# Optimization experiments

Measured on AMD Instinct MI355X. Metric: run time of the kernel, lower is better.

Reference implementation:

```python
import jax, jax.numpy as jnp
import numpy as np

NUM_LABELS = 32
EMB = 128          # label_embedding_dim
HID = 1024         # hidden_dim (== encoder feature dim)
B, S = 128, 512


def setup_inputs() -> dict:
    key = jax.random.key(0)
    ks = jax.random.split(key, 8)
    k = 1.0 / np.sqrt(HID)  # torch GRU/Linear default init bound
    u = lambda kk, shape: jax.random.uniform(kk, shape, jnp.float32, minval=-k, maxval=k)
    return {
        "hidden_states": jax.random.normal(ks[0], (B, S, HID), jnp.float32),
        "emb": jax.random.normal(ks[1], (NUM_LABELS, EMB), jnp.float32),  # nn.Embedding ~ N(0,1)
        "W_ih": u(ks[2], (3 * HID, EMB + HID)),  # GRU input weights, gate order r,z,n
        "W_hh": u(ks[3], (3 * HID, HID)),
        "b_ih": u(ks[4], (3 * HID,)),
        "b_hh": u(ks[5], (3 * HID,)),
        "W_out": u(ks[6], (NUM_LABELS, HID)),
        "b_out": u(ks[7], (NUM_LABELS,)),
    }


def reference(hidden_states, emb, W_ih, W_hh, b_ih, b_hh, W_out, b_out):
    batch = hidden_states.shape[0]
    h0 = jnp.zeros((batch, W_hh.shape[1]), hidden_states.dtype)
    lab0 = jnp.broadcast_to(emb[0], (batch, emb.shape[1]))  # label_start_embedding (id 0)

    def step(carry, x_t):
        h, lab = carry
        inp = jnp.concatenate([x_t, lab], axis=-1)            # [B, HID+EMB]
        gi = inp @ W_ih.T + b_ih                               # [B, 3*HID]
        gh = h @ W_hh.T + b_hh
        ir, iz, in_ = jnp.split(gi, 3, axis=-1)
        hr, hz, hn = jnp.split(gh, 3, axis=-1)
        r = jax.nn.sigmoid(ir + hr)
        z = jax.nn.sigmoid(iz + hz)
        n = jnp.tanh(in_ + r * hn)
        h_new = (1.0 - z) * n + z * h                          # PyTorch GRU update
        logit = h_new @ W_out.T + b_out                        # dropout is identity in eval
        pred = jnp.argmax(logit, axis=-1)                      # softmax is monotone; argmax(probs)==argmax(logit)
        return (h_new, emb[pred]), logit

    xs = jnp.swapaxes(hidden_states, 0, 1)                     # [S, B, HID]
    _, logits = jax.lax.scan(step, (h0, lab0), xs)             # logits: [S, B, L]
    return jnp.swapaxes(logits, 0, 1)                          # [B, S, L]
```

## Files before the change

### kernel.cpp

```cpp
#include <hip/hip_runtime.h>


#define S_    512
#define HID_  1024
#define EMB_  128
#define NL_   32
#define G3_   3072

#define LDS_A_STRIDE 1032
#define LDS_A_BYTES  (48 * LDS_A_STRIDE * 2)
#define CP_STRIDE    52
#define LDS_CP_BYTES (4 * 64 * CP_STRIDE * 4)
#define LDS_BYTES    (LDS_A_BYTES + LDS_CP_BYTES)

typedef __attribute__((ext_vector_type(8))) short          short8;
typedef __attribute__((ext_vector_type(8))) unsigned short u16x8;
typedef __attribute__((ext_vector_type(4))) unsigned short u16x4;
typedef __attribute__((ext_vector_type(4))) float          f32x4;
typedef unsigned long long u64_t;

__device__ unsigned int   g_ctr[576];
__device__ unsigned int   g_flag[1];
__device__ unsigned int   g_vis[256];
__device__ unsigned int   g_hseq[2][64 * 16];
__device__ unsigned int   g_predw[128 * 16];
__device__ unsigned short g_hhi[2][128 * HID_];
__device__ unsigned short g_hlo[2][128 * HID_];
__device__ float          g_hf32[2][128 * HID_];
__device__ float          g_Glab[NL_ * G3_];
__device__ unsigned short g_Wlox[G3_ * HID_];
__device__ unsigned short g_Wlohh[G3_ * HID_];
__device__ float          g_GIXall[(size_t)S_ * 128 * 64 * 48];

__device__ __forceinline__ float bf2f(unsigned short u) {
  union { unsigned int i; float f; } v; v.i = ((unsigned int)u) << 16; return v.f;
}
__device__ __forceinline__ unsigned short f2bf(float f) {
  union { float f; unsigned int i; } v; v.f = f;
  unsigned int u = v.i;
  return (unsigned short)((u + 0x7FFFu + ((u >> 16) & 1u)) >> 16);
}
__device__ __forceinline__ short8 ld_bf8(const unsigned short* p) {
  return __builtin_bit_cast(short8, *(const u16x8*)p);
}
__device__ __forceinline__ float ldin(const void* p, long i, int f32) {
  return f32 ? ((const float*)p)[i] : bf2f(((const unsigned short*)p)[i]);
}
__device__ __forceinline__ void store_out(void* out, int f32, long idx, float v) {
  if (f32) ((float*)out)[idx] = v;
  else     ((unsigned short*)out)[idx] = f2bf(v);
}

__device__ __forceinline__ u64_t ald64(const void* p) {
  return __hip_atomic_load((const u64_t*)p, __ATOMIC_RELAXED,
                           __HIP_MEMORY_SCOPE_AGENT);
}
__device__ __forceinline__ void ast64(void* p, u64_t v) {
  __hip_atomic_store((u64_t*)p, v, __ATOMIC_RELAXED,
                     __HIP_MEMORY_SCOPE_AGENT);
}
__device__ __forceinline__ unsigned int ald32(const unsigned int* p) {
  return __hip_atomic_load(p, __ATOMIC_RELAXED, __HIP_MEMORY_SCOPE_AGENT);
}
__device__ __forceinline__ void ast32(unsigned int* p, unsigned int v) {
  __hip_atomic_store(p, v, __ATOMIC_RELAXED, __HIP_MEMORY_SCOPE_AGENT);
}
__device__ __forceinline__ short8 ld_bf8_coh(const unsigned short* p) {
  union { u64_t q[2]; short8 s; } u;
  u.q[0] = ald64(p);
  u.q[1] = ald64(p + 4);
  return u.s;
}
__device__ __forceinline__ f32x4 ld_f4_coh(const float* p) {
  union { u64_t q[2]; f32x4 f; } u;
  u.q[0] = ald64(p);
  u.q[1] = ald64(p + 2);
  return u.f;
}
__device__ __forceinline__ void st_f4_coh(float* p, f32x4 v) {
  union { f32x4 f; u64_t q[2]; } u; u.f = v;
  ast64(p, u.q[0]);
  ast64(p + 2, u.q[1]);
}
__device__ __forceinline__ void st_h4_coh(unsigned short* p, u16x4 v) {
  union { u16x4 h; u64_t q; } u; u.h = v;
  ast64(p, u.q);
}

__global__ void k_zero() {
  int t = blockIdx.x * 256 + threadIdx.x;
  if (t < 576) g_ctr[t] = 0u;
  else if (t < 832) g_vis[t - 576] = 0u;
  if (t >= 2048 && t < 4096) ((unsigned int*)g_hseq)[t - 2048] = 0u;
  if (t >= 4096 && t < 6144) g_predw[t - 4096] = 0u;
  const u16x4 z4 = {0, 0, 0, 0};
  const f32x4 zf = {0.f, 0.f, 0.f, 0.f};
  for (int i = t; i < 2 * 128 * HID_ / 4; i += 65536) {
    ((u16x4*)g_hhi)[i] = z4;
    ((u16x4*)g_hlo)[i] = z4;
    ((f32x4*)g_hf32)[i] = zf;
  }
}

__global__ void k_detect(const unsigned short* __restrict__ W) {
  unsigned bad = 0;
  for (int i = threadIdx.x; i < 1024; i += 64) {
    float v = bf2f(W[i]);
    if (!(v * v <= 1.0f)) bad = 1;
  }
  unsigned long long b = __ballot(bad != 0);
  if (threadIdx.x == 0) g_flag[0] = (b != 0ull) ? 1u : 0u;
}

__global__ void k_prep(const void* __restrict__ emb,
                       const void* __restrict__ W_ih,
                       const void* __restrict__ b_ih) {
  const int f32 = (int)g_flag[0];
  int l = blockIdx.x / 12;
  int n = (blockIdx.x % 12) * 256 + threadIdx.x;
  double acc = (double)ldin(b_ih, n, f32);
  for (int e = 0; e < EMB_; ++e)
    acc += (double)ldin(emb, (long)l * EMB_ + e, f32) *
           (double)ldin(W_ih, (long)n * (HID_ + EMB_) + HID_ + e, f32);
  g_Glab[l * G3_ + n] = (float)acc;
}

__global__ void k_prepw(const void* __restrict__ W_ih,
                        const void* __restrict__ W_hh) {
  if (!g_flag[0]) return;
  long i4 = ((long)blockIdx.x * 256 + threadIdx.x) * 4;
  if (i4 >= (long)G3_ * HID_) return;
  int row = (int)(i4 >> 10), col = (int)(i4 & 1023);
  f32x4 wh = *(const f32x4*)&((const float*)W_hh)[(long)row * HID_ + col];
  f32x4 wx = *(const f32x4*)&((const float*)W_ih)[(long)row * (HID_ + EMB_) + col];
  u16x4 lh, lx;
  #pragma unroll
  for (int j = 0; j < 4; ++j) {
    unsigned short h1 = f2bf(wh[j]);
    lh[j] = f2bf(wh[j] - bf2f(h1));
    unsigned short x1 = f2bf(wx[j]);
    lx[j] = f2bf(wx[j] - bf2f(x1));
  }
  *(u16x4*)&g_Wlohh[i4] = lh;
  *(u16x4*)&g_Wlox[i4]  = lx;
}

__device__ __forceinline__ void gridbar(int wg, int bar) {
  __syncthreads();
  if (threadIdx.x == 0) {
    asm volatile("s_waitcnt vmcnt(0)" ::: "memory");
    unsigned int* c1   = g_ctr + (wg & 7) * 64;
    unsigned int* root = g_ctr + 512;
    unsigned int old = __hip_atomic_fetch_add(c1, 1u, __ATOMIC_RELAXED,
                                              __HIP_MEMORY_SCOPE_AGENT);
    if (old == 32u * (unsigned)(bar + 1) - 1u)
      __hip_atomic_fetch_add(root, 1u, __ATOMIC_RELAXED,
                             __HIP_MEMORY_SCOPE_AGENT);
    unsigned int tgt = 8u * (unsigned)(bar + 1);
    while (__hip_atomic_load(root, __ATOMIC_RELAXED,
                             __HIP_MEMORY_SCOPE_AGENT) < tgt)
      __builtin_amdgcn_s_sleep(1);
  }
  __syncthreads();
}

__device__ __forceinline__ void wait_hseq(int half, int it) {
  if (threadIdx.x < 64) {
    const unsigned int* p = &g_hseq[half][threadIdx.x * 16];
    while ((int)ald32(p) < it) { }
  }
  __builtin_amdgcn_sched_barrier(0);
  __syncthreads();
}

__device__ __forceinline__ void stage_w(unsigned short* sA, const void* Wsrc,
                                        int wstride, int rg, int f32, int tid) {
  if (f32) {
    const float* Ws = (const float*)Wsrc;
    for (int i = tid; i < 48 * 1024 / 4; i += 256) {
      int e = i * 4, row = e >> 10, k4 = e & 1023;
      int grow = (row >> 4) * HID_ + rg * 16 + (row & 15);
      f32x4 v = *(const f32x4*)&Ws[(long)grow * wstride + k4];
      u16x4 o;
      #pragma unroll
      for (int j = 0; j < 4; ++j) o[j] = f2bf(v[j]);
      *(u16x4*)&sA[row * LDS_A_STRIDE + k4] = o;
    }
  } else {
    const unsigned short* Ws = (const unsigned short*)Wsrc;
    for (int i = tid; i < 48 * 1024 / 4; i += 256) {
      int e = i * 4, row = e >> 10, k4 = e & 1023;
      int grow = (row >> 4) * HID_ + rg * 16 + (row & 15);
      *(u16x4*)&sA[row * LDS_A_STRIDE + k4] =
          *(const u16x4*)&Ws[(long)grow * wstride + k4];
    }
  }
}

__global__ __launch_bounds__(256) void k_seq(
    const void* __restrict__ hs,
    const void* __restrict__ W_ih,
    const void* __restrict__ W_hh,
    const void* __restrict__ b_hh,
    const void* __restrict__ W_out,
    const void* __restrict__ b_out,
    void* __restrict__ out) {
  extern __shared__ char smem[];
  unsigned short* sA  = (unsigned short*)smem;
  float*          sCp = (float*)(smem + LDS_A_BYTES);

  const int f32 = (int)g_flag[0];
  const int tid = threadIdx.x;
  const int wg  = blockIdx.x;
  const bool isx = (wg < 128);
  const int lid  = isx ? wg : wg - 128;
  const int rg = lid >> 1, bg = lid & 1;
  const int slot = lid;
  const int lane = tid & 63, wv = tid >> 6;
  const int m = lane & 15, q = lane >> 4;
  const int bl = tid & 63;
  const int jj = (tid >> 6) * 4;
  const int kw0 = wv * 256 + q * 8;

  int bar = 0;

  if (tid == 0) ast32(&g_vis[wg], (unsigned)wg + 1u);
  gridbar(wg, bar); ++bar;
  if (tid == 0) {
    unsigned p = ((unsigned)wg + 37u) & 255u;
    if (ald32(&g_vis[p]) != p + 1u) store_out(out, f32, wg, 999.0f);
  }

  {
    const int slot0 = wg & 127;
    const int rg0 = slot0 >> 1, bg0 = slot0 & 1;
    stage_w(sA, W_ih, HID_ + EMB_, rg0, f32, tid);
    __syncthreads();
    const long bstride = (long)S_ * HID_;
    const long boffb = (long)(bg0 * 64) * S_ * HID_;
    for (int t = 0; t < 256; ++t) {
      const int it = ((wg >> 7) << 8) | t;
      f32x4 acc[3][4];
      #pragma unroll
      for (int rt = 0; rt < 3; ++rt)
        #pragma unroll
        for (int bt = 0; bt < 4; ++bt) acc[rt][bt] = f32x4{0.f, 0.f, 0.f, 0.f};
      const long boff = boffb + (long)it * HID_;
      if (f32) {
        const float* Bf = (const float*)hs + boff;
        #pragma unroll
        for (int kb = 0; kb < 8; ++kb) {
          const int k = kw0 + kb * 32;
          short8 avh[3];
          #pragma unroll
          for (int rt = 0; rt < 3; ++rt)
            avh[rt] = ld_bf8(&sA[(rt * 16 + m) * LDS_A_STRIDE + k]);
          short8 bxh[4], bxl[4];
          #pragma unroll
          for (int bt = 0; bt < 4; ++bt) {
            const float* bp = Bf + (long)(bt * 16 + m) * bstride + k;
            f32x4 x0 = *(const f32x4*)bp;
            f32x4 x1 = *(const f32x4*)(bp + 4);
            u16x8 th, tl;
            #pragma unroll
            for (int j = 0; j < 4; ++j) {
              unsigned short u0 = f2bf(x0[j]);
              th[j] = u0; tl[j] = f2bf(x0[j] - bf2f(u0));
              unsigned short u1 = f2bf(x1[j]);
              th[4 + j] = u1; tl[4 + j] = f2bf(x1[j] - bf2f(u1));
            }
            bxh[bt] = __builtin_bit_cast(short8, th);
            bxl[bt] = __builtin_bit_cast(short8, tl);
          }
          short8 avl[3];
          #pragma unroll
          for (int rt = 0; rt < 3; ++rt)
            avl[rt] = ld_bf8(&g_Wlox[(long)(rt * HID_ + rg0 * 16 + m) * HID_ + k]);
          #pragma unroll
          for (int rt = 0; rt < 3; ++rt)
            #pragma unroll
            for (int bt = 0; bt < 4; ++bt) {
              acc[rt][bt] = __builtin_amdgcn_mfma_f32_16x16x32_bf16(
                  avh[rt], bxh[bt], acc[rt][bt], 0, 0, 0);
              acc[rt][bt] = __builtin_amdgcn_mfma_f32_16x16x32_bf16(
                  avh[rt], bxl[bt], acc[rt][bt], 0, 0, 0);
              acc[rt][bt] = __builtin_amdgcn_mfma_f32_16x16x32_bf16(
                  avl[rt], bxh[bt], acc[rt][bt], 0, 0, 0);
              acc[rt][bt] = __builtin_amdgcn_mfma_f32_16x16x32_bf16(
                  avl[rt], bxl[bt], acc[rt][bt], 0, 0, 0);
            }
        }
      } else {
        const unsigned short* Bh = (const unsigned short*)hs + boff;
        #pragma unroll
        for (int kb = 0; kb < 8; ++kb) {
          const int k = kw0 + kb * 32;
          short8 avh[3], bxh[4];
          #pragma unroll
          for (int rt = 0; rt < 3; ++rt)
            avh[rt] = ld_bf8(&sA[(rt * 16 + m) * LDS_A_STRIDE + k]);
          #pragma unroll
          for (int bt = 0; bt < 4; ++bt)
            bxh[bt] = ld_bf8(&Bh[(long)(bt * 16 + m) * bstride + k]);
          #pragma unroll
          for (int rt = 0; rt < 3; ++rt)
            #pragma unroll
            for (int bt = 0; bt < 4; ++bt)
              acc[rt][bt] = __builtin_amdgcn_mfma_f32_16x16x32_bf16(
                  avh[rt], bxh[bt], acc[rt][bt], 0, 0, 0);
        }
      }
      __syncthreads();
      #pragma unroll
      for (int rt = 0; rt < 3; ++rt)
        #pragma unroll
        for (int bt = 0; bt < 4; ++bt)
          *(f32x4*)&sCp[(wv * 64 + bt * 16 + m) * CP_STRIDE + rt * 16 + q * 4] =
              acc[rt][bt];
      __syncthreads();
      #pragma unroll
      for (int g = 0; g < 3; ++g) {
        f32x4 sv = f32x4{0.f, 0.f, 0.f, 0.f};
        #pragma unroll
        for (int w = 0; w < 4; ++w)
          sv += *(const f32x4*)&sCp[(w * 64 + bl) * CP_STRIDE + g * 16 + jj];
        *(f32x4*)&g_GIXall[(((long)it * 128 + slot0) * 64 + bl) * 48 +
                           g * 16 + jj] = sv;
      }
      __syncthreads();
    }
  }
  __threadfence();
  gridbar(wg, bar); ++bar;

  if (!isx) stage_w(sA, W_hh, HID_, rg, f32, tid);
  __syncthreads();

  float bo = 0.f;
  if (isx && tid < 32) bo = ldin(b_out, tid, f32);
  f32x4 bhh[3];
  if (!isx) {
    const int jbase = rg * 16 + jj;
    #pragma unroll
    for (int g = 0; g < 3; ++g)
      #pragma unroll
      for (int t = 0; t < 4; ++t)
        bhh[g][t] = ldin(b_hh, (long)g * HID_ + jbase + t, f32);
  }

  float hreg[4] = {0.f, 0.f, 0.f, 0.f};
  f32x4 sred[3];

  for (int it = 0; it <= S_; ++it) {
    if (isx && it >= 1) {
      wait_hseq(wg >> 6, it);
      const int rb = (it + 1) & 1;
      if (it == 1 && wg == 0 && tid == 0) {
        float s = 0.f;
        for (int i = 0; i < 16; ++i) {
          union { u64_t q; float f[2]; } u; u.q = ald64(&g_hf32[0][2 * i]);
          s += u.f[0] * u.f[0] + u.f[1] * u.f[1];
        }
        if (s == 0.f) store_out(out, f32, 300, 555.0f);
      }
      const int b = wg, s = it - 1;
      float* scrp  = sCp;
      float* shrow = sCp + 256;
      {
        f32x4 hv = ld_f4_coh(&g_hf32[rb][(long)b * HID_ + tid * 4]);
        *(f32x4*)&shrow[(tid >> 5) * 132 + (tid & 31) * 4] = hv;
      }
      __syncthreads();
      {
        int l = tid >> 3, kc = tid & 7;
        const float* hr = shrow + kc * 132;
        float p = 0.f;
        if (f32) {
          const float* wr = (const float*)W_out + (long)l * HID_ + kc * 128;
          for (int k = 0; k < 128; k += 4) {
            f32x4 wa = *(const f32x4*)&wr[k];
            f32x4 ha = *(const f32x4*)&hr[k];
            #pragma unroll
            for (int j = 0; j < 4; ++j) p += wa[j] * ha[j];
          }
        } else {
          const unsigned short* wr =
              (const unsigned short*)W_out + (long)l * HID_ + kc * 128;
          for (int k = 0; k < 128; k += 8) {
            u16x8 w8 = *(const u16x8*)&wr[k];
            f32x4 ha = *(const f32x4*)&hr[k];
            f32x4 hb = *(const f32x4*)&hr[k + 4];
            #pragma unroll
            for (int j = 0; j < 4; ++j) {
              p += bf2f(w8[j]) * ha[j];
              p += bf2f(w8[4 + j]) * hb[j];
            }
          }
        }
        scrp[tid] = p;
      }
      __syncthreads();
      if (tid < 32) {
        const float* pp = sCp + tid * 8;
        float v = pp[0] + pp[1] + pp[2] + pp[3] + pp[4] + pp[5] + pp[6] + pp[7]
                  + bo;
        store_out(out, f32, ((long)b * S_ + s) * NL_ + tid, v);
        float bv = v; int bi = tid;
        #pragma unroll
        for (int off = 16; off; off >>= 1) {
          float v2 = __shfl_down(bv, off, 32);
          int   i2 = __shfl_down(bi, off, 32);
          if (v2 > bv || (v2 == bv && i2 < bi)) { bv = v2; bi = i2; }
        }
        if (tid == 0) ast32(&g_predw[b * 16], ((unsigned)it << 8) | (unsigned)bi);
      }
      __syncthreads();
    }

    if (!isx && it < S_) {
      f32x4 gixp[3];
      #pragma unroll
      for (int g = 0; g < 3; ++g)
        gixp[g] = *(const f32x4*)&g_GIXall[(((long)it * 128 + slot) * 64 + bl)
                                           * 48 + g * 16 + jj];

      wait_hseq(bg, it);
      const int rb = (it + 1) & 1;
      const int wb = it & 1;

      f32x4 acc[3][4];
      #pragma unroll
      for (int rt = 0; rt < 3; ++rt)
        #pragma unroll
        for (int bt = 0; bt < 4; ++bt) acc[rt][bt] = f32x4{0.f, 0.f, 0.f, 0.f};

      const unsigned short* Bhi = g_hhi[rb] + (long)(bg * 64) * HID_;
      const unsigned short* Blo = g_hlo[rb] + (long)(bg * 64) * HID_;
      #pragma unroll
      for (int kb = 0; kb < 8; ++kb) {
        const int k = kw0 + kb * 32;
        short8 avh[3], bh[4], blv[4];
        #pragma unroll
        for (int rt = 0; rt < 3; ++rt)
          avh[rt] = ld_bf8(&sA[(rt * 16 + m) * LDS_A_STRIDE + k]);
        #pragma unroll
        for (int bt = 0; bt < 4; ++bt) {
          bh[bt]  = ld_bf8_coh(&Bhi[(long)(bt * 16 + m) * HID_ + k]);
          blv[bt] = ld_bf8_coh(&Blo[(long)(bt * 16 + m) * HID_ + k]);
        }
        #pragma unroll
        for (int rt = 0; rt < 3; ++rt)
          #pragma unroll
          for (int bt = 0; bt < 4; ++bt) {
            acc[rt][bt] = __builtin_amdgcn_mfma_f32_16x16x32_bf16(
                avh[rt], bh[bt], acc[rt][bt], 0, 0, 0);
            acc[rt][bt] = __builtin_amdgcn_mfma_f32_16x16x32_bf16(
                avh[rt], blv[bt], acc[rt][bt], 0, 0, 0);
          }
        if (f32) {
          short8 avl[3];
          #pragma unroll
          for (int rt = 0; rt < 3; ++rt)
            avl[rt] = ld_bf8(&g_Wlohh[(long)(rt * HID_ + rg * 16 + m) * HID_ + k]);
          #pragma unroll
          for (int rt = 0; rt < 3; ++rt)
            #pragma unroll
            for (int bt = 0; bt < 4; ++bt) {
              acc[rt][bt] = __builtin_amdgcn_mfma_f32_16x16x32_bf16(
                  avl[rt], bh[bt], acc[rt][bt], 0, 0, 0);
              acc[rt][bt] = __builtin_amdgcn_mfma_f32_16x16x32_bf16(
                  avl[rt], blv[bt], acc[rt][bt], 0, 0, 0);
            }
        }
      }

      __syncthreads();
      #pragma unroll
      for (int rt = 0; rt < 3; ++rt)
        #pragma unroll
        for (int bt = 0; bt < 4; ++bt)
          *(f32x4*)&sCp[(wv * 64 + bt * 16 + m) * CP_STRIDE + rt * 16 + q * 4] =
              acc[rt][bt];
      __syncthreads();
      #pragma unroll
      for (int g = 0; g < 3; ++g) {
        f32x4 sv = f32x4{0.f, 0.f, 0.f, 0.f};
        #pragma unroll
        for (int w = 0; w < 4; ++w)
          sv += *(const f32x4*)&sCp[(w * 64 + bl) * CP_STRIDE + g * 16 + jj];
        sred[g] = sv;
      }

      const int bglob = bg * 64 + bl;
      int pb = 0;
      if (it >= 1) {
        const unsigned int* pw = &g_predw[bglob * 16];
        unsigned w = ald32(pw);
        while ((int)(w >> 8) < it) { w = ald32(pw); }
        pb = (int)(w & 255u);
      }
      __builtin_amdgcn_sched_barrier(0);

      const int jbase = rg * 16 + jj;
      const float* gl = g_Glab + (long)pb * G3_;
      f32x4 glab[3];
      #pragma unroll
      for (int g = 0; g < 3; ++g)
        glab[g] = *(const f32x4*)&gl[g * HID_ + jbase];
      u16x4 whi, wlo;
      f32x4 hf;
      #pragma unroll
      for (int t4 = 0; t4 < 4; ++t4) {
        float ghr = sred[0][t4] + bhh[0][t4];
        float ghz = sred[1][t4] + bhh[1][t4];
        float ghn = sred[2][t4] + bhh[2][t4];
        float gir = gixp[0][t4] + glab[0][t4];
        float giz = gixp[1][t4] + glab[1][t4];
        float gin = gixp[2][t4] + glab[2][t4];
        float r = 1.f / (1.f + expf(-(gir + ghr)));
        float z = 1.f / (1.f + expf(-(giz + ghz)));
        float n = tanhf(gin + r * ghn);
        float hn = (1.f - z) * n + z * hreg[t4];
        hreg[t4] = hn;
        hf[t4] = hn;
        unsigned short uhi = f2bf(hn);
        whi[t4] = uhi;
        wlo[t4] = f2bf(hn - bf2f(uhi));
      }
      st_h4_coh(&g_hhi[wb][(long)bglob * HID_ + jbase], whi);
      st_h4_coh(&g_hlo[wb][(long)bglob * HID_ + jbase], wlo);
      st_f4_coh(&g_hf32[wb][(long)bglob * HID_ + jbase], hf);

      asm volatile("s_waitcnt vmcnt(0)" ::: "memory");
      __syncthreads();
      if (tid == 0) ast32(&g_hseq[bg][rg * 16], (unsigned)(it + 1));
    }
  }
}

extern "C" void kernel_launch(void* const* d_in, const int* in_sizes, int n_in,
                              void* d_out, int out_size, void* d_ws, size_t ws_size,
                              hipStream_t stream) {
  const void* hs    = d_in[0];
  const void* emb   = d_in[1];
  const void* W_ih  = d_in[2];
  const void* W_hh  = d_in[3];
  const void* b_ih  = d_in[4];
  const void* b_hh  = d_in[5];
  const void* W_out = d_in[6];
  const void* b_out = d_in[7];

  hipLaunchKernelGGL(k_zero, dim3(256), dim3(256), 0, stream);
  hipLaunchKernelGGL(k_detect, dim3(1), dim3(64), 0, stream,
                     (const unsigned short*)W_ih);
  hipLaunchKernelGGL(k_prep, dim3(32 * 12), dim3(256), 0, stream,
                     emb, W_ih, b_ih);
  hipLaunchKernelGGL(k_prepw, dim3(3072), dim3(256), 0, stream, W_ih, W_hh);
  hipFuncSetAttribute((const void*)k_seq,
                      hipFuncAttributeMaxDynamicSharedMemorySize, LDS_BYTES);
  hipLaunchKernelGGL(k_seq, dim3(256), dim3(256), LDS_BYTES, stream,
                     hs, W_ih, W_hh, b_hh, W_out, b_out, d_out);
}
```

Before: 17.11 ms.

## Fuse output-projection partial sums into GRU workgroups, drop fp32 hidden state buffer

Each hidden-state workgroup now holds its 16-column slice of W_out in LDS and computes partial logits for its hidden slice right after the GRU update. It writes these per-slice partials to a global buffer instead of the full fp32 hidden state. The output workgroups then only sum 64 partials per label rather than reading a 1024-wide row and running the whole projection. This moves projection work off the critical serial chain and removes the fp32 hidden-state traffic, at the cost of an extra LDS reduction and barriers in the recurrent workgroups.

Measured after the change: 16.98 ms. Within noise of the previous version (-0.8%).

```diff
diff --git a/kernel.cpp b/kernel.cpp
--- a/kernel.cpp
+++ b/kernel.cpp
@@ -11,7 +11,8 @@
 #define LDS_A_BYTES  (48 * LDS_A_STRIDE * 2)
 #define CP_STRIDE    52
 #define LDS_CP_BYTES (4 * 64 * CP_STRIDE * 4)
-#define LDS_BYTES    (LDS_A_BYTES + LDS_CP_BYTES)
+#define LDS_WO_BYTES 2048
+#define LDS_BYTES    (LDS_A_BYTES + LDS_CP_BYTES + LDS_WO_BYTES)
 
 typedef __attribute__((ext_vector_type(8))) short          short8;
 typedef __attribute__((ext_vector_type(8))) unsigned short u16x8;
@@ -26,7 +27,7 @@
 __device__ unsigned int   g_predw[128 * 16];
 __device__ unsigned short g_hhi[2][128 * HID_];
 __device__ unsigned short g_hlo[2][128 * HID_];
-__device__ float          g_hf32[2][128 * HID_];
+__device__ float          g_lp[64 * 128 * 32];
 __device__ float          g_Glab[NL_ * G3_];
 __device__ unsigned short g_Wlox[G3_ * HID_];
 __device__ unsigned short g_Wlohh[G3_ * HID_];
@@ -61,6 +62,12 @@
 }
 __device__ __forceinline__ unsigned int ald32(const unsigned int* p) {
   return __hip_atomic_load(p, __ATOMIC_RELAXED, __HIP_MEMORY_SCOPE_AGENT);
+}
+__device__ __forceinline__ float aldf(const float* p) {
+  union { unsigned int u; float f; } v;
+  v.u = __hip_atomic_load((const unsigned int*)p, __ATOMIC_RELAXED,
+                          __HIP_MEMORY_SCOPE_AGENT);
+  return v.f;
 }
 __device__ __forceinline__ void ast32(unsigned int* p, unsigned int v) {
   __hip_atomic_store(p, v, __ATOMIC_RELAXED, __HIP_MEMORY_SCOPE_AGENT);
@@ -71,19 +78,12 @@
   u.q[1] = ald64(p + 4);
   return u.s;
 }
-__device__ __forceinline__ f32x4 ld_f4_coh(const float* p) {
-  union { u64_t q[2]; f32x4 f; } u;
-  u.q[0] = ald64(p);
-  u.q[1] = ald64(p + 2);
-  return u.f;
-}
-__device__ __forceinline__ void st_f4_coh(float* p, f32x4 v) {
-  union { f32x4 f; u64_t q[2]; } u; u.f = v;
-  ast64(p, u.q[0]);
-  ast64(p + 2, u.q[1]);
-}
 __device__ __forceinline__ void st_h4_coh(unsigned short* p, u16x4 v) {
   union { u16x4 h; u64_t q; } u; u.h = v;
+  ast64(p, u.q);
+}
+__device__ __forceinline__ void st_f2_coh(float* p, float a, float b) {
+  union { float f[2]; u64_t q; } u; u.f[0] = a; u.f[1] = b;
   ast64(p, u.q);
 }
 
@@ -94,11 +94,9 @@
   if (t >= 2048 && t < 4096) ((unsigned int*)g_hseq)[t - 2048] = 0u;
   if (t >= 4096 && t < 6144) g_predw[t - 4096] = 0u;
   const u16x4 z4 = {0, 0, 0, 0};
-  const f32x4 zf = {0.f, 0.f, 0.f, 0.f};
   for (int i = t; i < 2 * 128 * HID_ / 4; i += 65536) {
     ((u16x4*)g_hhi)[i] = z4;
     ((u16x4*)g_hlo)[i] = z4;
-    ((f32x4*)g_hf32)[i] = zf;
   }
 }
 
@@ -208,6 +206,7 @@
   extern __shared__ char smem[];
   unsigned short* sA  = (unsigned short*)smem;
   float*          sCp = (float*)(smem + LDS_A_BYTES);
+  float*          sWo = (float*)(smem + LDS_A_BYTES + LDS_CP_BYTES);
 
   const int f32 = (int)g_flag[0];
   const int tid = threadIdx.x;
@@ -333,7 +332,13 @@
   __threadfence();
   gridbar(wg, bar); ++bar;
 
-  if (!isx) stage_w(sA, W_hh, HID_, rg, f32, tid);
+  if (!isx) {
+    stage_w(sA, W_hh, HID_, rg, f32, tid);
+    for (int i = tid; i < NL_ * 16; i += 256) {
+      int l = i >> 4, tt = i & 15;
+      sWo[i] = ldin(W_out, (long)l * HID_ + rg * 16 + tt, f32);
+    }
+  }
   __syncthreads();
 
   float bo = 0.f;
@@ -354,56 +359,27 @@
   for (int it = 0; it <= S_; ++it) {
     if (isx && it >= 1) {
       wait_hseq(wg >> 6, it);
-      const int rb = (it + 1) & 1;
       if (it == 1 && wg == 0 && tid == 0) {
-        float s = 0.f;
-        for (int i = 0; i < 16; ++i) {
-          union { u64_t q; float f[2]; } u; u.q = ald64(&g_hf32[0][2 * i]);
-          s += u.f[0] * u.f[0] + u.f[1] * u.f[1];
-        }
-        if (s == 0.f) store_out(out, f32, 300, 555.0f);
+        u64_t a = ald64(&g_hhi[0][0]) | ald64(&g_hhi[0][4]) |
+                  ald64(&g_hhi[0][8]) | ald64(&g_hhi[0][12]);
+        if (a == 0ull) store_out(out, f32, 300, 555.0f);
       }
       const int b = wg, s = it - 1;
-      float* scrp  = sCp;
-      float* shrow = sCp + 256;
       {
-        f32x4 hv = ld_f4_coh(&g_hf32[rb][(long)b * HID_ + tid * 4]);
-        *(f32x4*)&shrow[(tid >> 5) * 132 + (tid & 31) * 4] = hv;
-      }
-      __syncthreads();
-      {
-        int l = tid >> 3, kc = tid & 7;
-        const float* hr = shrow + kc * 132;
+        int l = tid & 31, c = tid >> 5;
         float p = 0.f;
-        if (f32) {
-          const float* wr = (const float*)W_out + (long)l * HID_ + kc * 128;
-          for (int k = 0; k < 128; k += 4) {
-            f32x4 wa = *(const f32x4*)&wr[k];
-            f32x4 ha = *(const f32x4*)&hr[k];
-            #pragma unroll
-            for (int j = 0; j < 4; ++j) p += wa[j] * ha[j];
-          }
-        } else {
-          const unsigned short* wr =
-              (const unsigned short*)W_out + (long)l * HID_ + kc * 128;
-          for (int k = 0; k < 128; k += 8) {
-            u16x8 w8 = *(const u16x8*)&wr[k];
-            f32x4 ha = *(const f32x4*)&hr[k];
-            f32x4 hb = *(const f32x4*)&hr[k + 4];
-            #pragma unroll
-            for (int j = 0; j < 4; ++j) {
-              p += bf2f(w8[j]) * ha[j];
-              p += bf2f(w8[4 + j]) * hb[j];
-            }
-          }
-        }
-        scrp[tid] = p;
+        #pragma unroll
+        for (int j = 0; j < 8; ++j)
+          p += aldf(&g_lp[(((c * 8 + j) * 128) + b) * 32 + l]);
+        sCp[l * 8 + c] = p;
       }
       __syncthreads();
       if (tid < 32) {
         const float* pp = sCp + tid * 8;
-        float v = pp[0] + pp[1] + pp[2] + pp[3] + pp[4] + pp[5] + pp[6] + pp[7]
-                  + bo;
+        float v = pp[0];
+        v += pp[1]; v += pp[2]; v += pp[3];
+        v += pp[4]; v += pp[5]; v += pp[6]; v += pp[7];
+        v += bo;
         store_out(out, f32, ((long)b * S_ + s) * NL_ + tid, v);
         float bv = v; int bi = tid;
         #pragma unroll
@@ -490,6 +466,7 @@
           sv += *(const f32x4*)&sCp[(w * 64 + bl) * CP_STRIDE + g * 16 + jj];
         sred[g] = sv;
       }
+      __syncthreads();
 
       const int bglob = bg * 64 + bl;
       int pb = 0;
@@ -508,7 +485,6 @@
       for (int g = 0; g < 3; ++g)
         glab[g] = *(const f32x4*)&gl[g * HID_ + jbase];
       u16x4 whi, wlo;
-      f32x4 hf;
       #pragma unroll
       for (int t4 = 0; t4 < 4; ++t4) {
         float ghr = sred[0][t4] + bhh[0][t4];
@@ -522,14 +498,43 @@
         float n = tanhf(gin + r * ghn);
         float hn = (1.f - z) * n + z * hreg[t4];
         hreg[t4] = hn;
-        hf[t4] = hn;
         unsigned short uhi = f2bf(hn);
         whi[t4] = uhi;
         wlo[t4] = f2bf(hn - bf2f(uhi));
       }
       st_h4_coh(&g_hhi[wb][(long)bglob * HID_ + jbase], whi);
       st_h4_coh(&g_hlo[wb][(long)bglob * HID_ + jbase], wlo);
-      st_f4_coh(&g_hf32[wb][(long)bglob * HID_ + jbase], hf);
+
+      #pragma unroll
+      for (int l0 = 0; l0 < 32; l0 += 4) {
+        f32x4 pv;
+        #pragma unroll
+        for (int dl = 0; dl < 4; ++dl) {
+          const float* wv4 = &sWo[(l0 + dl) * 16 + jj];
+          float pl = wv4[0] * hreg[0];
+          pl += wv4[1] * hreg[1];
+          pl += wv4[2] * hreg[2];
+          pl += wv4[3] * hreg[3];
+          pv[dl] = pl;
+        }
+        *(f32x4*)&sCp[tid * 32 + l0] = pv;
+      }
+      __syncthreads();
+      {
+        const int b2 = tid >> 2, l0 = (tid & 3) * 8;
+        f32x4 s0 = *(const f32x4*)&sCp[(0 * 64 + b2) * 32 + l0];
+        f32x4 s1 = *(const f32x4*)&sCp[(0 * 64 + b2) * 32 + l0 + 4];
+        #pragma unroll
+        for (int w = 1; w < 4; ++w) {
+          s0 += *(const f32x4*)&sCp[(w * 64 + b2) * 32 + l0];
+          s1 += *(const f32x4*)&sCp[(w * 64 + b2) * 32 + l0 + 4];
+        }
+        float* lp = &g_lp[((long)rg * 128 + bg * 64 + b2) * 32 + l0];
+        st_f2_coh(lp + 0, s0[0], s0[1]);
+        st_f2_coh(lp + 2, s0[2], s0[3]);
+        st_f2_coh(lp + 4, s1[0], s1[1]);
+        st_f2_coh(lp + 6, s1[2], s1[3]);
+      }
 
       asm volatile("s_waitcnt vmcnt(0)" ::: "memory");
       __syncthreads();
```
